# Performance work log

Measured on AMD Instinct MI355X. Metric: run time of the kernel, lower is better.

## Reference

```python
import jax, jax.numpy as jnp
import numpy as np

VOCAB_SIZE = 250002
UNUSED_TOKEN_IDS = np.array([0, 2, 1, 3])  # cls, eos, pad, unk (XLM-R tokenizer)
EPS = 1e-12


def _l2norm(x):
    n = jnp.sqrt(jnp.sum(x * x, axis=-1, keepdims=True))
    return x / jnp.maximum(n, EPS)


def setup_inputs() -> dict:
    key = jax.random.key(0)
    k1, k2, k3, k4 = jax.random.split(key, 4)
    B, S, H = 16, 2048, 1024
    hidden_state = jax.random.normal(k1, (B, S, H), dtype=jnp.float32)
    attention_mask = jnp.ones((B, S), dtype=jnp.float32)
    input_ids = jax.random.randint(k2, (B, S), 0, VOCAB_SIZE, dtype=jnp.int64)
    sparse_W = jax.random.normal(k3, (H, 1), dtype=jnp.float32) * 0.02
    sparse_b = jnp.zeros((1,), dtype=jnp.float32)
    colbert_W = jax.random.normal(k4, (H, H), dtype=jnp.float32) * 0.02
    colbert_b = jnp.zeros((H,), dtype=jnp.float32)
    return {
        "hidden_state": hidden_state,
        "attention_mask": attention_mask,
        "input_ids": input_ids,
        "sparse_W": sparse_W,
        "sparse_b": sparse_b,
        "colbert_W": colbert_W,
        "colbert_b": colbert_b,
    }


def reference(hidden_state, attention_mask, input_ids, sparse_W, sparse_b, colbert_W, colbert_b):
    B, S, H = hidden_state.shape
    # dense vector: CLS token, L2-normalized
    dense_vecs = _l2norm(hidden_state[:, 0])  # (B, H)

    # sparse: relu(Linear(H,1)) per token, scatter into vocab, max over seq.
    # scatter into zeros(B,S,V) + max over dim=1 == per-batch scatter-max into (B,V)
    token_weights = jax.nn.relu(
        jnp.einsum("bsh,ho->bso", hidden_state, sparse_W) + sparse_b
    )[..., 0]  # (B, S)
    batch_idx = jnp.arange(B)[:, None]  # (B, 1)
    sparse_vecs = jnp.zeros((B, VOCAB_SIZE), dtype=token_weights.dtype)
    sparse_vecs = sparse_vecs.at[batch_idx, input_ids].max(token_weights)
    # zero out special tokens (cls/eos/pad/unk)
    sparse_vecs = sparse_vecs.at[:, jnp.asarray(UNUSED_TOKEN_IDS)].set(0.0)

    # colbert: Linear(H,H) on tokens 1:, masked, then L2-normalized
    colbert_vecs = jnp.einsum("bsh,hd->bsd", hidden_state[:, 1:], colbert_W) + colbert_b
    colbert_vecs = colbert_vecs * attention_mask[:, 1:, None]
    colbert_vecs = _l2norm(colbert_vecs)  # (B, S-1, H)

    return dense_vecs, sparse_vecs, colbert_vecs
```

## Files before the change

### kernel.cpp

```cpp
#include <hip/hip_runtime.h>
#include <hip/hip_bf16.h>

#define HDIM 1024
#define SEQ  2048
#define BATCH 16
#define VOCAB 250002
#define M_TOT (BATCH * SEQ)
#define SPARSE_OFF (BATCH * HDIM)
#define COLBERT_OFF (SPARSE_OFF + BATCH * VOCAB)

typedef __attribute__((ext_vector_type(8))) short short8;
typedef __attribute__((ext_vector_type(4))) float f32x4;

static __device__ __forceinline__ unsigned short f2bf(float f) {
  union { float f; unsigned u; } v; v.f = f;
  unsigned r = v.u + 0x7fffu + ((v.u >> 16) & 1u);
  return (unsigned short)(r >> 16);
}

static __device__ __forceinline__ void gll16(const unsigned short* g, unsigned short* l) {
  __builtin_amdgcn_global_load_lds(
      (const __attribute__((address_space(1))) unsigned int*)g,
      (__attribute__((address_space(3))) unsigned int*)l, 16, 0, 0);
}

__global__ __launch_bounds__(256) void prep_kernel(
    const float* __restrict__ W, unsigned short* __restrict__ Wt,
    float* __restrict__ out, const float* __restrict__ hidden)
{
  __shared__ float tile[32][33];
  __shared__ float red[4];
  const int blk = blockIdx.x;
  if (blk < 1024) {
    const int n0 = (blk & 31) * 32, k0 = (blk >> 5) * 32;
    const int tx = threadIdx.x & 31, ty = threadIdx.x >> 5;
#pragma unroll
    for (int i = ty; i < 32; i += 8)
      tile[i][tx] = W[(size_t)(k0 + i) * HDIM + n0 + tx];
    __syncthreads();
#pragma unroll
    for (int i = ty; i < 32; i += 8)
      Wt[(size_t)(n0 + i) * HDIM + k0 + tx] = f2bf(tile[tx][i]);
  } else if (blk < 1536) {
    float4 z = {0.f, 0.f, 0.f, 0.f};
    float4* p = (float4*)(out + SPARSE_OFF);
    int idx = (blk - 1024) * 256 + threadIdx.x;
#pragma unroll 1
    for (; idx < 1000008; idx += 512 * 256) p[idx] = z;
  } else {
    const int b = blk - 1536;
    const int t = threadIdx.x;
    const float4* x = (const float4*)(hidden + (size_t)b * SEQ * HDIM);
    float4 v = x[t];
    float ss = v.x * v.x + v.y * v.y + v.z * v.z + v.w * v.w;
#pragma unroll
    for (int off = 32; off; off >>= 1) ss += __shfl_down(ss, off);
    if ((t & 63) == 0) red[t >> 6] = ss;
    __syncthreads();
    float tot = red[0] + red[1] + red[2] + red[3];
    float inv = 1.0f / fmaxf(sqrtf(tot), 1e-12f);
    v.x *= inv; v.y *= inv; v.z *= inv; v.w *= inv;
    ((float4*)(out + (size_t)b * HDIM))[t] = v;
  }
}

__global__ __launch_bounds__(256) void cast_sparse_kernel(
    const float* __restrict__ hidden,
    const float* __restrict__ sparse_W,
    const float* __restrict__ sparse_b,
    const int* __restrict__ input_ids,
    unsigned short* __restrict__ hidden_bf,
    float* __restrict__ sparse_out)
{
  const int token = blockIdx.x * 4 + (threadIdx.x >> 6);
  const int lane = threadIdx.x & 63;

  const float4* xr = (const float4*)(hidden + (size_t)token * HDIM);
  const float4* wr = (const float4*)sparse_W;
  ushort4* hb = (ushort4*)(hidden_bf + (size_t)token * HDIM);

  float dot = 0.0f;
#pragma unroll
  for (int i = 0; i < 4; i++) {
    const int idx = i * 64 + lane;
    float4 xv = xr[idx];
    float4 wv = wr[idx];
    dot = fmaf(xv.x, wv.x, dot);
    dot = fmaf(xv.y, wv.y, dot);
    dot = fmaf(xv.z, wv.z, dot);
    dot = fmaf(xv.w, wv.w, dot);
    ushort4 o;
    o.x = f2bf(xv.x); o.y = f2bf(xv.y); o.z = f2bf(xv.z); o.w = f2bf(xv.w);
    hb[idx] = o;
  }
#pragma unroll
  for (int off = 32; off; off >>= 1) dot += __shfl_down(dot, off);

  if (lane == 0) {
    float w = dot + sparse_b[0];
    if (w > 0.0f) {
      int id = input_ids[token];
      if (id > 3) {
        int b = token >> 11;
        atomicMax((int*)(sparse_out + (size_t)b * VOCAB + id), __float_as_int(w));
      }
    }
  }
}

#define BS_ELEMS (1024 * 32)
#define AS_ELEMS (64 * 32)
#define LDS_BYTES ((2 * BS_ELEMS + 2 * AS_ELEMS) * 2)

__global__ __launch_bounds__(512, 2) void gemm_norm_kernel(
    const unsigned short* __restrict__ Abf,
    const unsigned short* __restrict__ Btbf,
    const float* __restrict__ bias,
    const float* __restrict__ mask,
    float* __restrict__ out)
{
  extern __shared__ __align__(16) char smem[];
  unsigned short* Bs0 = (unsigned short*)smem;
  unsigned short* Bs1 = Bs0 + BS_ELEMS;
  unsigned short* As0 = Bs1 + BS_ELEMS;
  unsigned short* As1 = As0 + AS_ELEMS;
  float* redLDS = (float*)smem;
  float* invLDS = (float*)smem + 64 * 8;

  const int t = threadIdx.x;
  const int wv = t >> 6, l = t & 63;
  const int q = l >> 4, ml = l & 15;
  const int mBase = blockIdx.x * 64;

  int boff[8];
#pragma unroll
  for (int c = 0; c < 8; c++) {
    int cb = c * 512 + wv * 64 + l;
    int n = cb >> 2;
    int kc = ((cb & 3) - (n >> 1)) & 3;
    boff[c] = n * HDIM + kc * 8;
  }
  int aoff;
  {
    int ca = wv * 64 + l;
    int row = ca >> 2;
    int kc = ((ca & 3) - (row >> 1)) & 3;
    aoff = (mBase + row) * HDIM + kc * 8;
  }

  f32x4 acc[4][8] = {};

#define STAGE(K0, BD, AD)                                               \
  do {                                                                  \
    _Pragma("unroll")                                                   \
    for (int c = 0; c < 8; c++)                                         \
      gll16(Btbf + boff[c] + (K0), (BD) + (c * 512 + wv * 64) * 8);     \
    if (wv < 4) gll16(Abf + aoff + (K0), (AD) + (wv * 64) * 8);         \
  } while (0)

  STAGE(0, Bs0, As0);
  __syncthreads();

  for (int kk = 0; kk < 32; kk++) {
    unsigned short* Bc = (kk & 1) ? Bs1 : Bs0;
    unsigned short* Ac = (kk & 1) ? As1 : As0;
    if (kk < 31) {
      unsigned short* Bn = (kk & 1) ? Bs0 : Bs1;
      unsigned short* An = (kk & 1) ? As0 : As1;
      STAGE((kk + 1) * 32, Bn, An);
    }

    short8 af[4], bf[4];
#pragma unroll
    for (int i = 0; i < 4; i++) {
      const int ar = i * 16 + ml;
      af[i] = *(const short8*)(Ac + ar * 32 + (((q + (ar >> 1)) & 3) * 8));
    }
#pragma unroll
    for (int jh = 0; jh < 2; jh++) {
#pragma unroll
      for (int jj = 0; jj < 4; jj++) {
        const int br = wv * 128 + (jh * 4 + jj) * 16 + ml;
        bf[jj] = *(const short8*)(Bc + br * 32 + (((q + (br >> 1)) & 3) * 8));
      }
#pragma unroll
      for (int i = 0; i < 4; i++)
#pragma unroll
        for (int jj = 0; jj < 4; jj++)
          acc[i][jh * 4 + jj] =
              __builtin_amdgcn_mfma_f32_16x16x32_bf16(af[i], bf[jj], acc[i][jh * 4 + jj], 0, 0, 0);
    }
    __syncthreads();
  }

  float bv[8];
#pragma unroll
  for (int j = 0; j < 8; j++) bv[j] = bias[wv * 128 + j * 16 + ml];
#pragma unroll
  for (int i = 0; i < 4; i++)
#pragma unroll
    for (int j = 0; j < 8; j++)
#pragma unroll
      for (int r = 0; r < 4; r++) acc[i][j][r] += bv[j];

#pragma unroll
  for (int i = 0; i < 4; i++) {
#pragma unroll
    for (int r = 0; r < 4; r++) {
      float ss = 0.0f;
#pragma unroll
      for (int j = 0; j < 8; j++) { float x = acc[i][j][r]; ss = fmaf(x, x, ss); }
      ss += __shfl_xor(ss, 1); ss += __shfl_xor(ss, 2);
      ss += __shfl_xor(ss, 4); ss += __shfl_xor(ss, 8);
      if (ml == 0) redLDS[(i * 16 + q * 4 + r) * 8 + wv] = ss;
    }
  }
  __syncthreads();

  {
    const int row = t >> 3, w = t & 7;
    float v = redLDS[row * 8 + w];
    v += __shfl_xor(v, 1); v += __shfl_xor(v, 2); v += __shfl_xor(v, 4);
    if (w == 0) {
      const int gm = mBase + row;
      const int s = gm & (SEQ - 1), b = gm >> 11;
      const float mval = mask[b * SEQ + s];
      invLDS[row] = mval / fmaxf(fabsf(mval) * sqrtf(v), 1e-12f);
    }
  }
  __syncthreads();

#pragma unroll
  for (int i = 0; i < 4; i++) {
#pragma unroll
    for (int r = 0; r < 4; r++) {
      const int row = i * 16 + q * 4 + r;
      const int gm = mBase + row;
      const int s = gm & (SEQ - 1);
      if (s != 0) {
        const int b = gm >> 11;
        float* orow = out + COLBERT_OFF + (size_t)(b * (SEQ - 1) + s - 1) * HDIM;
        const float iv = invLDS[row];
#pragma unroll
        for (int j = 0; j < 8; j++)
          orow[wv * 128 + j * 16 + ml] = acc[i][j][r] * iv;
      }
    }
  }
}

extern "C" void kernel_launch(void* const* d_in, const int* in_sizes, int n_in,
                              void* d_out, int out_size, void* d_ws, size_t ws_size,
                              hipStream_t stream) {
  (void)in_sizes; (void)n_in; (void)out_size; (void)ws_size;
  const float* hidden = (const float*)d_in[0];
  const float* attn_mask = (const float*)d_in[1];
  const int* input_ids = (const int*)d_in[2];
  const float* sparse_W = (const float*)d_in[3];
  const float* sparse_b = (const float*)d_in[4];
  const float* colbert_W = (const float*)d_in[5];
  const float* colbert_b = (const float*)d_in[6];
  float* out = (float*)d_out;

  unsigned short* hidden_bf = (unsigned short*)d_ws;
  unsigned short* Wt = (unsigned short*)((char*)d_ws + (size_t)M_TOT * HDIM * 2);

  prep_kernel<<<1552, 256, 0, stream>>>(colbert_W, Wt, out, hidden);
  cast_sparse_kernel<<<M_TOT / 4, 256, 0, stream>>>(
      hidden, sparse_W, sparse_b, input_ids, hidden_bf, out + SPARSE_OFF);
  gemm_norm_kernel<<<M_TOT / 64, 512, LDS_BYTES, stream>>>(
      hidden_bf, Wt, colbert_b, attn_mask, out);
}
```

Measured before the change: 375.4 us.

## Fuse bf16 cast and sparse scoring into GEMM, read B fragments directly from global

Merges the cast/sparse kernel into the GEMM kernel. Each block now converts its 64 fp32 rows to bf16 straight into LDS while computing the sparse dot and atomicMax, which removes the bf16 hidden-state round trip through global memory and one launch. The colbert weight is pre-packed into an MFMA fragment layout so each wave loads its B fragments directly from global/L2 into registers, with a manual software pipeline over K, instead of staging B through double-buffered LDS. Output stores become nontemporal. The risk is that B now depends on L2/global latency per wave and the block's cast prologue is not overlapped with compute.

```diff
diff --git a/kernel.cpp b/kernel.cpp
--- a/kernel.cpp
+++ b/kernel.cpp
@@ -1,5 +1,4 @@
 #include <hip/hip_runtime.h>
-#include <hip/hip_bf16.h>
 
 #define HDIM 1024
 #define SEQ  2048
@@ -16,12 +15,6 @@
   union { float f; unsigned u; } v; v.f = f;
   unsigned r = v.u + 0x7fffu + ((v.u >> 16) & 1u);
   return (unsigned short)(r >> 16);
-}
-
-static __device__ __forceinline__ void gll16(const unsigned short* g, unsigned short* l) {
-  __builtin_amdgcn_global_load_lds(
-      (const __attribute__((address_space(1))) unsigned int*)g,
-      (__attribute__((address_space(3))) unsigned int*)l, 16, 0, 0);
 }
 
 __global__ __launch_bounds__(256) void prep_kernel(
@@ -39,8 +32,12 @@
       tile[i][tx] = W[(size_t)(k0 + i) * HDIM + n0 + tx];
     __syncthreads();
 #pragma unroll
-    for (int i = ty; i < 32; i += 8)
-      Wt[(size_t)(n0 + i) * HDIM + k0 + tx] = f2bf(tile[tx][i]);
+    for (int i = ty; i < 32; i += 8) {
+      const int n = n0 + i, k = k0 + tx;
+      const size_t idx = (size_t)((n >> 4) * 32 + (k >> 5)) * 512
+                       + (size_t)((((k >> 3) & 3) * 16 + (n & 15)) * 8 + (k & 7));
+      Wt[idx] = f2bf(tile[tx][i]);
+    }
   } else if (blk < 1536) {
     float4 z = {0.f, 0.f, 0.f, 0.f};
     float4* p = (float4*)(out + SPARSE_OFF);
@@ -64,138 +61,129 @@
   }
 }
 
-__global__ __launch_bounds__(256) void cast_sparse_kernel(
+#define FUSED_LDS (64 * HDIM * 2 + (64 * 8 + 64) * 4)
+
+__global__ __launch_bounds__(512, 2) void fused_kernel(
     const float* __restrict__ hidden,
+    const unsigned short* __restrict__ Bp,
+    const float* __restrict__ bias,
+    const float* __restrict__ mask,
     const float* __restrict__ sparse_W,
     const float* __restrict__ sparse_b,
     const int* __restrict__ input_ids,
-    unsigned short* __restrict__ hidden_bf,
-    float* __restrict__ sparse_out)
-{
-  const int token = blockIdx.x * 4 + (threadIdx.x >> 6);
-  const int lane = threadIdx.x & 63;
-
-  const float4* xr = (const float4*)(hidden + (size_t)token * HDIM);
-  const float4* wr = (const float4*)sparse_W;
-  ushort4* hb = (ushort4*)(hidden_bf + (size_t)token * HDIM);
-
-  float dot = 0.0f;
-#pragma unroll
-  for (int i = 0; i < 4; i++) {
-    const int idx = i * 64 + lane;
-    float4 xv = xr[idx];
-    float4 wv = wr[idx];
-    dot = fmaf(xv.x, wv.x, dot);
-    dot = fmaf(xv.y, wv.y, dot);
-    dot = fmaf(xv.z, wv.z, dot);
-    dot = fmaf(xv.w, wv.w, dot);
-    ushort4 o;
-    o.x = f2bf(xv.x); o.y = f2bf(xv.y); o.z = f2bf(xv.z); o.w = f2bf(xv.w);
-    hb[idx] = o;
-  }
-#pragma unroll
-  for (int off = 32; off; off >>= 1) dot += __shfl_down(dot, off);
-
-  if (lane == 0) {
-    float w = dot + sparse_b[0];
-    if (w > 0.0f) {
-      int id = input_ids[token];
-      if (id > 3) {
-        int b = token >> 11;
-        atomicMax((int*)(sparse_out + (size_t)b * VOCAB + id), __float_as_int(w));
-      }
-    }
-  }
-}
-
-#define BS_ELEMS (1024 * 32)
-#define AS_ELEMS (64 * 32)
-#define LDS_BYTES ((2 * BS_ELEMS + 2 * AS_ELEMS) * 2)
-
-__global__ __launch_bounds__(512, 2) void gemm_norm_kernel(
-    const unsigned short* __restrict__ Abf,
-    const unsigned short* __restrict__ Btbf,
-    const float* __restrict__ bias,
-    const float* __restrict__ mask,
     float* __restrict__ out)
 {
   extern __shared__ __align__(16) char smem[];
-  unsigned short* Bs0 = (unsigned short*)smem;
-  unsigned short* Bs1 = Bs0 + BS_ELEMS;
-  unsigned short* As0 = Bs1 + BS_ELEMS;
-  unsigned short* As1 = As0 + AS_ELEMS;
-  float* redLDS = (float*)smem;
-  float* invLDS = (float*)smem + 64 * 8;
+  unsigned short* As = (unsigned short*)smem;
+  float* redLDS = (float*)(smem + 64 * HDIM * 2);
+  float* invLDS = redLDS + 64 * 8;
 
   const int t = threadIdx.x;
-  const int wv = t >> 6, l = t & 63;
+  const int w = t >> 6, l = t & 63;
   const int q = l >> 4, ml = l & 15;
   const int mBase = blockIdx.x * 64;
 
-  int boff[8];
-#pragma unroll
-  for (int c = 0; c < 8; c++) {
-    int cb = c * 512 + wv * 64 + l;
-    int n = cb >> 2;
-    int kc = ((cb & 3) - (n >> 1)) & 3;
-    boff[c] = n * HDIM + kc * 8;
-  }
-  int aoff;
   {
-    int ca = wv * 64 + l;
-    int row = ca >> 2;
-    int kc = ((ca & 3) - (row >> 1)) & 3;
-    aoff = (mBase + row) * HDIM + kc * 8;
-  }
+    const float sb = sparse_b[0];
+    for (int r8 = 0; r8 < 8; r8++) {
+      const int row = w * 8 + r8;
+      const int gm = mBase + row;
+      const float* src = hidden + (size_t)gm * HDIM;
+      float dot = 0.f;
+#pragma unroll
+      for (int c = 0; c < 2; c++) {
+        const int k0 = c * 512 + l * 8;
+        f32x4 x0 = __builtin_nontemporal_load((const f32x4*)(src + k0));
+        f32x4 x1 = __builtin_nontemporal_load((const f32x4*)(src + k0) + 1);
+        const f32x4 w0 = *((const f32x4*)(sparse_W + k0));
+        const f32x4 w1 = *((const f32x4*)(sparse_W + k0) + 1);
+        dot = fmaf(x0.x, w0.x, dot); dot = fmaf(x0.y, w0.y, dot);
+        dot = fmaf(x0.z, w0.z, dot); dot = fmaf(x0.w, w0.w, dot);
+        dot = fmaf(x1.x, w1.x, dot); dot = fmaf(x1.y, w1.y, dot);
+        dot = fmaf(x1.z, w1.z, dot); dot = fmaf(x1.w, w1.w, dot);
+        short8 o;
+        o[0] = (short)f2bf(x0.x); o[1] = (short)f2bf(x0.y);
+        o[2] = (short)f2bf(x0.z); o[3] = (short)f2bf(x0.w);
+        o[4] = (short)f2bf(x1.x); o[5] = (short)f2bf(x1.y);
+        o[6] = (short)f2bf(x1.z); o[7] = (short)f2bf(x1.w);
+        const int kk = k0 >> 5;
+        const int slot = (((k0 >> 3) & 3) + (row >> 1)) & 3;
+        const int byte = (kk * 4096 + row * 64 + slot * 16) ^ ((kk & 1) << 6);
+        *(short8*)(smem + byte) = o;
+      }
+#pragma unroll
+      for (int off = 32; off; off >>= 1) dot += __shfl_down(dot, off);
+      if (l == 0) {
+        const float wgt = dot + sb;
+        if (wgt > 0.f) {
+          const int id = input_ids[gm];
+          if (id > 3) {
+            const int b = gm >> 11;
+            atomicMax((int*)(out + SPARSE_OFF + (size_t)b * VOCAB + id),
+                      __float_as_int(wgt));
+          }
+        }
+      }
+    }
+  }
+  __syncthreads();
+
+  int aoff[4];
+#pragma unroll
+  for (int i = 0; i < 4; i++) {
+    const int ar = i * 16 + ml;
+    aoff[i] = ar * 64 + (((q + (ar >> 1)) & 3) * 16);
+  }
+  const unsigned short* Bpw = Bp + (size_t)(w * 8 * 32) * 512 + l * 8;
 
   f32x4 acc[4][8] = {};
-
-#define STAGE(K0, BD, AD)                                               \
-  do {                                                                  \
-    _Pragma("unroll")                                                   \
-    for (int c = 0; c < 8; c++)                                         \
-      gll16(Btbf + boff[c] + (K0), (BD) + (c * 512 + wv * 64) * 8);     \
-    if (wv < 4) gll16(Abf + aoff + (K0), (AD) + (wv * 64) * 8);         \
+  short8 aC[4], aN[4], b0[4], b1[4];
+
+#define LOADA(dst, KK) do {                                              \
+    const int fl_ = ((KK) & 1) << 6;                                     \
+    const int kb_ = (KK) * 4096;                                         \
+    _Pragma("unroll")                                                    \
+    for (int i_ = 0; i_ < 4; i_++)                                       \
+      dst[i_] = *(const short8*)(smem + ((aoff[i_] ^ fl_) + kb_));       \
   } while (0)
 
-  STAGE(0, Bs0, As0);
-  __syncthreads();
-
-  for (int kk = 0; kk < 32; kk++) {
-    unsigned short* Bc = (kk & 1) ? Bs1 : Bs0;
-    unsigned short* Ac = (kk & 1) ? As1 : As0;
-    if (kk < 31) {
-      unsigned short* Bn = (kk & 1) ? Bs0 : Bs1;
-      unsigned short* An = (kk & 1) ? As0 : As1;
-      STAGE((kk + 1) * 32, Bn, An);
-    }
-
-    short8 af[4], bf[4];
-#pragma unroll
-    for (int i = 0; i < 4; i++) {
-      const int ar = i * 16 + ml;
-      af[i] = *(const short8*)(Ac + ar * 32 + (((q + (ar >> 1)) & 3) * 8));
-    }
-#pragma unroll
-    for (int jh = 0; jh < 2; jh++) {
-#pragma unroll
-      for (int jj = 0; jj < 4; jj++) {
-        const int br = wv * 128 + (jh * 4 + jj) * 16 + ml;
-        bf[jj] = *(const short8*)(Bc + br * 32 + (((q + (br >> 1)) & 3) * 8));
-      }
-#pragma unroll
-      for (int i = 0; i < 4; i++)
-#pragma unroll
-        for (int jj = 0; jj < 4; jj++)
-          acc[i][jh * 4 + jj] =
-              __builtin_amdgcn_mfma_f32_16x16x32_bf16(af[i], bf[jj], acc[i][jh * 4 + jj], 0, 0, 0);
-    }
-    __syncthreads();
+#define LOADB(dst, JOFS, KK) do {                                        \
+    _Pragma("unroll")                                                    \
+    for (int j_ = 0; j_ < 4; j_++)                                       \
+      dst[j_] = *(const short8*)(Bpw +                                   \
+          (size_t)(((j_ + (JOFS)) * 32 + (KK)) * 512));                  \
+  } while (0)
+
+#define MF(AF, BF, JB) do {                                              \
+    _Pragma("unroll")                                                    \
+    for (int i_ = 0; i_ < 4; i_++)                                       \
+      _Pragma("unroll")                                                  \
+      for (int j_ = 0; j_ < 4; j_++)                                     \
+        acc[i_][(JB) + j_] = __builtin_amdgcn_mfma_f32_16x16x32_bf16(    \
+            AF[i_], BF[j_], acc[i_][(JB) + j_], 0, 0, 0);                \
+  } while (0)
+
+  LOADA(aC, 0);
+  LOADB(b0, 0, 0);
+
+#pragma unroll 1
+  for (int kk = 0; kk < 32; kk += 2) {
+    LOADB(b1, 4, kk);
+    LOADA(aN, kk + 1);
+    MF(aC, b0, 0);
+    LOADB(b0, 0, kk + 1);
+    MF(aC, b1, 4);
+    const int k2 = (kk + 2) & 31;
+    LOADB(b1, 4, kk + 1);
+    LOADA(aC, k2);
+    MF(aN, b0, 0);
+    LOADB(b0, 0, k2);
+    MF(aN, b1, 4);
   }
 
   float bv[8];
 #pragma unroll
-  for (int j = 0; j < 8; j++) bv[j] = bias[wv * 128 + j * 16 + ml];
+  for (int j = 0; j < 8; j++) bv[j] = bias[w * 128 + j * 16 + ml];
 #pragma unroll
   for (int i = 0; i < 4; i++)
 #pragma unroll
@@ -212,16 +200,16 @@
       for (int j = 0; j < 8; j++) { float x = acc[i][j][r]; ss = fmaf(x, x, ss); }
       ss += __shfl_xor(ss, 1); ss += __shfl_xor(ss, 2);
       ss += __shfl_xor(ss, 4); ss += __shfl_xor(ss, 8);
-      if (ml == 0) redLDS[(i * 16 + q * 4 + r) * 8 + wv] = ss;
+      if (ml == 0) redLDS[(i * 16 + q * 4 + r) * 8 + w] = ss;
     }
   }
   __syncthreads();
 
   {
-    const int row = t >> 3, w = t & 7;
-    float v = redLDS[row * 8 + w];
+    const int row = t >> 3, wp = t & 7;
+    float v = redLDS[row * 8 + wp];
     v += __shfl_xor(v, 1); v += __shfl_xor(v, 2); v += __shfl_xor(v, 4);
-    if (w == 0) {
+    if (wp == 0) {
       const int gm = mBase + row;
       const int s = gm & (SEQ - 1), b = gm >> 11;
       const float mval = mask[b * SEQ + s];
@@ -243,7 +231,8 @@
         const float iv = invLDS[row];
 #pragma unroll
         for (int j = 0; j < 8; j++)
-          orow[wv * 128 + j * 16 + ml] = acc[i][j][r] * iv;
+          __builtin_nontemporal_store(acc[i][j][r] * iv,
+                                      orow + w * 128 + j * 16 + ml);
       }
     }
   }
@@ -262,12 +251,9 @@
   const float* colbert_b = (const float*)d_in[6];
   float* out = (float*)d_out;
 
-  unsigned short* hidden_bf = (unsigned short*)d_ws;
-  unsigned short* Wt = (unsigned short*)((char*)d_ws + (size_t)M_TOT * HDIM * 2);
+  unsigned short* Wt = (unsigned short*)d_ws;
 
   prep_kernel<<<1552, 256, 0, stream>>>(colbert_W, Wt, out, hidden);
-  cast_sparse_kernel<<<M_TOT / 4, 256, 0, stream>>>(
-      hidden, sparse_W, sparse_b, input_ids, hidden_bf, out + SPARSE_OFF);
-  gemm_norm_kernel<<<M_TOT / 64, 512, LDS_BYTES, stream>>>(
-      hidden_bf, Wt, colbert_b, attn_mask, out);
-}
+  fused_kernel<<<M_TOT / 64, 512, FUSED_LDS, stream>>>(
+      hidden, Wt, colbert_b, attn_mask, sparse_W, sparse_b, input_ids, out);
+}
```

Result: faster. 335.8 us (-10.6%).
